# Kernel tuning notes

Measured on AMD Instinct MI355X. Metric: run time of the kernel, lower is better.

## Reference

```python
import jax, jax.numpy as jnp
import numpy as np

DIM = 384
B, H, W = 32, 32, 32


def setup_inputs() -> dict:
    key = jax.random.key(0)
    ks = jax.random.split(key, 10)
    s = 1.0 / np.sqrt(DIM)  # conv-like init scale
    return {
        "rgb_feat": jax.random.normal(ks[0], (B, DIM, H, W), dtype=jnp.float32),
        "ms_feat": jax.random.normal(ks[1], (B, DIM, H, W), dtype=jnp.float32),
        "Wq": jax.random.normal(ks[2], (DIM, DIM), dtype=jnp.float32) * s,
        "bq": jax.random.normal(ks[3], (DIM,), dtype=jnp.float32) * s,
        "Wk": jax.random.normal(ks[4], (DIM, DIM), dtype=jnp.float32) * s,
        "bk": jax.random.normal(ks[5], (DIM,), dtype=jnp.float32) * s,
        "Wv": jax.random.normal(ks[6], (DIM, DIM), dtype=jnp.float32) * s,
        "bv": jax.random.normal(ks[7], (DIM,), dtype=jnp.float32) * s,
        "Wf": jax.random.normal(ks[8], (DIM, DIM), dtype=jnp.float32) * s,
        "bf": jax.random.normal(ks[9], (DIM,), dtype=jnp.float32) * s,
    }


def _proj(x_bcn, Wdc, b_d):
    # 1x1 conv == channel-mixing linear: (b,c,n) -> (b,d,n)
    return jnp.einsum('dc,bcn->bdn', Wdc, x_bcn) + b_d[None, :, None]


def reference(rgb_feat, ms_feat, Wq, bq, Wk, bk, Wv, bv, Wf, bf):
    b, c, h, w = rgb_feat.shape
    n = h * w
    rgb = rgb_feat.reshape(b, c, n)
    ms = ms_feat.reshape(b, c, n)

    q = _proj(rgb, Wq, bq)   # (b, c, n)
    k = _proj(ms, Wk, bk)    # (b, c, n)
    v = _proj(ms, Wv, bv)    # (b, c, n)

    scale = 1.0 / jnp.sqrt(jnp.asarray(c, dtype=q.dtype))
    # scores: (b, n_q, n_k) == bmm(q^T, k) / sqrt(c)
    scores = jnp.einsum('bcn,bcm->bnm', q, k) * scale
    attn = jax.nn.softmax(scores, axis=-1)
    # out: (b, n, c) == bmm(attn, v^T); back to (b, c, n)
    out = jnp.einsum('bnm,bcm->bcn', attn, v)

    fused = _proj(out, Wf, bf)  # final 1x1 conv
    return fused.reshape(b, c, h, w)
```

## Files before the change

### kernel.cpp

```cpp
#include <hip/hip_runtime.h>

#define DIMC 384
#define NTOK 1024
#define BATCH 32
#define KT12 12

using short8 = __attribute__((ext_vector_type(8))) short;
using f32x4  = __attribute__((ext_vector_type(4))) float;
using uint4_ = __attribute__((ext_vector_type(4))) unsigned int;
typedef unsigned short u16;

#define MFMA16 __builtin_amdgcn_mfma_f32_16x16x32_bf16

#define GLD_LDS16(gp, lp)                                                     \
    __builtin_amdgcn_global_load_lds(                                         \
        (const __attribute__((address_space(1))) void*)(gp),                  \
        (__attribute__((address_space(3))) void*)(lp), 16, 0, 0)

__device__ __forceinline__ u16 f2bf(float f) {
    unsigned int u = __builtin_bit_cast(unsigned int, f);
    u += 0x7FFFu + ((u >> 16) & 1u);
    return (u16)(u >> 16);
}
__device__ __forceinline__ float bf2f(u16 h) {
    unsigned int u = ((unsigned int)h) << 16;
    return __builtin_bit_cast(float, u);
}


__global__ __launch_bounds__(256) void transpose_sw(
    const float* __restrict__ X0, u16* __restrict__ X0sw,
    const float* __restrict__ X1, u16* __restrict__ X1sw)
{
    __shared__ float tl[64 * 65];
    const int z = blockIdx.z;
    const float* X = (z < BATCH) ? X0 : X1;
    u16* Xsw = (z < BATCH) ? X0sw : X1sw;
    const int b = z & 31, n0 = blockIdx.x * 64, c0 = blockIdx.y * 64;
    const int t = threadIdx.x;

#pragma unroll
    for (int p = 0; p < 4; ++p) {
        int idx = p * 256 + t;
        int c = idx >> 4, n4 = (idx & 15) * 4;
        f32x4 v = *(const f32x4*)(X + ((size_t)b * DIMC + c0 + c) * NTOK + n0 + n4);
#pragma unroll
        for (int i = 0; i < 4; ++i) tl[c * 65 + n4 + i] = v[i];
    }
    __syncthreads();
    u16* dstb = Xsw + (size_t)b * NTOK * DIMC;
#pragma unroll
    for (int p = 0; p < 2; ++p) {
        int g = p * 256 + t;
        int n15 = g & 15, quad = (g >> 4) & 3, ktl = (g >> 6) & 1, rg = g >> 7;
        int c8 = ktl * 32 + quad * 8;
        int nl = rg * 16 + n15;
        uint4_ pk;
#pragma unroll
        for (int i = 0; i < 4; ++i) {
            u16 lo = f2bf(tl[(c8 + 2 * i) * 65 + nl]);
            u16 hi = f2bf(tl[(c8 + 2 * i + 1) * 65 + nl]);
            pk[i] = (unsigned)lo | ((unsigned)hi << 16);
        }
        size_t dst = (((size_t)(n0 >> 4) + rg) * KT12 + (c0 >> 5) + ktl) * 512 + (size_t)(g & 63) * 8;
        *(uint4_*)(dstb + dst) = pk;
    }
}

__global__ __launch_bounds__(256) void wcvt_sw(
    const float* __restrict__ w0, const float* __restrict__ w1,
    const float* __restrict__ w2, const float* __restrict__ w3,
    u16* __restrict__ dst, float s0)
{
    const float* srcs[4] = {w0, w1, w2, w3};
    const float* s = srcs[blockIdx.y];
    float scl = (blockIdx.y == 0) ? s0 : 1.0f;
    u16* d = dst + (size_t)blockIdx.y * DIMC * DIMC;
    int e0 = (blockIdx.x * 256 + threadIdx.x) * 8;
    int dd = e0 / DIMC, c8 = e0 % DIMC;
    f32x4 a = *(const f32x4*)(s + e0);
    f32x4 b2 = *(const f32x4*)(s + e0 + 4);
    uint4_ pk;
    pk[0] = (unsigned)f2bf(a[0] * scl) | ((unsigned)f2bf(a[1] * scl) << 16);
    pk[1] = (unsigned)f2bf(a[2] * scl) | ((unsigned)f2bf(a[3] * scl) << 16);
    pk[2] = (unsigned)f2bf(b2[0] * scl) | ((unsigned)f2bf(b2[1] * scl) << 16);
    pk[3] = (unsigned)f2bf(b2[2] * scl) | ((unsigned)f2bf(b2[3] * scl) << 16);
    size_t off = ((size_t)(dd >> 4) * KT12 + (c8 >> 5)) * 512 +
                 (size_t)((((c8 >> 3) & 3) * 16 + (dd & 15)) * 8);
    *(uint4_*)(d + off) = pk;
}

__global__ __launch_bounds__(256, 4) void proj3_g(
    const u16* __restrict__ rgb_sw, const u16* __restrict__ ms_sw,
    const u16* __restrict__ w_sw,
    u16* __restrict__ q_sw, u16* __restrict__ k_sw, u16* __restrict__ v_sw,
    const float* __restrict__ bq, const float* __restrict__ bk,
    const float* __restrict__ bv, float s0)
{
    __shared__ __align__(16) u16 smem[16384];

    const int bid = blockIdx.x;
    const int b = bid & 31;
    const int rr = bid >> 5;
    const int s = rr % 3, tile = rr / 3;
    const size_t TB = (size_t)NTOK * DIMC, WN = (size_t)DIMC * DIMC;
    const u16 *A, *B; u16* O; const float* bias;
    int ktd, bRow, r0, c0; float bsc = 1.f;
    if (s == 0) {
        A = rgb_sw + b * TB; B = w_sw; O = q_sw + b * TB; bias = bq;
        ktd = 12; bRow = 0; r0 = (tile & 7) * 128; c0 = (tile >> 3) * 128; bsc = s0;
    } else if (s == 1) {
        A = ms_sw + b * TB; B = w_sw + WN; O = k_sw + b * TB; bias = bk;
        ktd = 12; bRow = 0; r0 = (tile & 7) * 128; c0 = (tile >> 3) * 128;
    } else {
        A = w_sw + 2 * WN; B = ms_sw + b * TB; O = v_sw + b * TB; bias = bv;
        ktd = 32; bRow = 1; r0 = (tile % 3) * 128; c0 = (tile / 3) * 128;
    }

    const int t = threadIdx.x, w = t >> 6, lane = t & 63;
    const int l15 = lane & 15, quad = lane >> 4;
    const int wr = w >> 1, wc = w & 1;
    const int rt0 = r0 >> 4, ct0 = c0 >> 4;

    f32x4 acc[4][4];
#pragma unroll
    for (int ai = 0; ai < 4; ++ai)
#pragma unroll
        for (int bj = 0; bj < 4; ++bj) acc[ai][bj] = (f32x4){0.f, 0.f, 0.f, 0.f};

    {
        const u16* As = A + ((size_t)(rt0 + 2 * w) * KT12) * 512 + (size_t)lane * 8;
        GLD_LDS16(As, smem + (2 * w) * 512);
        GLD_LDS16(As + KT12 * 512, smem + (2 * w + 1) * 512);
        const u16* Bs = B + ((size_t)(ct0 + 2 * w) * KT12) * 512 + (size_t)lane * 8;
        GLD_LDS16(Bs, smem + 8192 + (2 * w) * 512);
        GLD_LDS16(Bs + KT12 * 512, smem + 8192 + (2 * w + 1) * 512);
    }
    __syncthreads();

    for (int kt = 0; kt < 12; ++kt) {
        const int cur = kt & 1;
        if (kt < 11) {
            u16* dA = smem + (cur ^ 1) * 4096;
            u16* dB = smem + 8192 + (cur ^ 1) * 4096;
            const u16* As = A + ((size_t)(rt0 + 2 * w) * KT12 + kt + 1) * 512 + (size_t)lane * 8;
            GLD_LDS16(As, dA + (2 * w) * 512);
            GLD_LDS16(As + KT12 * 512, dA + (2 * w + 1) * 512);
            const u16* Bs = B + ((size_t)(ct0 + 2 * w) * KT12 + kt + 1) * 512 + (size_t)lane * 8;
            GLD_LDS16(Bs, dB + (2 * w) * 512);
            GLD_LDS16(Bs + KT12 * 512, dB + (2 * w + 1) * 512);
        }
        const u16* sA = smem + cur * 4096 + (size_t)(wr * 4) * 512 + (size_t)lane * 8;
        const u16* sB = smem + 8192 + cur * 4096 + (size_t)(wc * 4) * 512 + (size_t)lane * 8;
        short8 aF[4], bF[4];
#pragma unroll
        for (int ai = 0; ai < 4; ++ai) aF[ai] = *(const short8*)(sA + ai * 512);
#pragma unroll
        for (int bj = 0; bj < 4; ++bj) bF[bj] = *(const short8*)(sB + bj * 512);
        __builtin_amdgcn_s_setprio(1);
#pragma unroll
        for (int ai = 0; ai < 4; ++ai)
#pragma unroll
            for (int bj = 0; bj < 4; ++bj)
                acc[ai][bj] = MFMA16(aF[ai], bF[bj], acc[ai][bj], 0, 0, 0);
        __builtin_amdgcn_s_setprio(0);
        __syncthreads();
    }
    u16* pw = smem + w * 1216;

    if (bRow) {
#pragma unroll
        for (int ai = 0; ai < 4; ++ai) {
            f32x4 bv4 = *(const f32x4*)(bias + r0 + wr * 64 + ai * 16 + quad * 4);
#pragma unroll
            for (int bj = 0; bj < 4; ++bj)
#pragma unroll
                for (int r = 0; r < 4; ++r) acc[ai][bj][r] += bv4[r];
        }
    } else {
#pragma unroll
        for (int bj = 0; bj < 4; ++bj) {
            float bc = bias[c0 + wc * 64 + bj * 16 + l15] * bsc;
#pragma unroll
            for (int ai = 0; ai < 4; ++ai)
#pragma unroll
                for (int r = 0; r < 4; ++r) acc[ai][bj][r] += bc;
        }
    }

#pragma unroll
    for (int ai = 0; ai < 4; ++ai) {
#pragma unroll
        for (int bj = 0; bj < 4; ++bj)
#pragma unroll
            for (int r = 0; r < 4; ++r)
                pw[(quad * 4 + r) * 76 + bj * 16 + l15] = f2bf(acc[ai][bj][r]);
        const int rt = rt0 + wr * 4 + ai;
        const int kb0 = (c0 + wc * 64) >> 5;
#pragma unroll
        for (int ktl = 0; ktl < 2; ++ktl) {
            uint4_ v = *(const uint4_*)(pw + l15 * 76 + ktl * 32 + quad * 8);
            *(uint4_*)(O + ((size_t)rt * ktd + kb0 + ktl) * 512 + (size_t)lane * 8) = v;
        }
    }
}

__global__ __launch_bounds__(256, 4) void projf_g(
    const u16* __restrict__ wf_sw, const u16* __restrict__ osw,
    const float* __restrict__ bfp, float* __restrict__ out)
{
    __shared__ __align__(16) u16 smem[16384];
    const int bid = blockIdx.x;
    const int b = bid & 31, tile = bid >> 5;
    const int r0 = (tile % 3) * 128, c0 = (tile / 3) * 128;
    const size_t TB = (size_t)NTOK * DIMC;

    const int t = threadIdx.x, w = t >> 6, lane = t & 63;
    const int l15 = lane & 15, quad = lane >> 4;
    const int wr = w >> 1, wc = w & 1;
    const int rt0 = r0 >> 4, ct0 = c0 >> 4;
    const u16* A = wf_sw;
    const u16* B = osw + (size_t)b * TB;

    f32x4 acc[4][4];
#pragma unroll
    for (int ai = 0; ai < 4; ++ai)
#pragma unroll
        for (int bj = 0; bj < 4; ++bj) acc[ai][bj] = (f32x4){0.f, 0.f, 0.f, 0.f};

    {
        const u16* As = A + ((size_t)(rt0 + 2 * w) * KT12) * 512 + (size_t)lane * 8;
        GLD_LDS16(As, smem + (2 * w) * 512);
        GLD_LDS16(As + KT12 * 512, smem + (2 * w + 1) * 512);
        const u16* Bs = B + ((size_t)(ct0 + 2 * w) * KT12) * 512 + (size_t)lane * 8;
        GLD_LDS16(Bs, smem + 8192 + (2 * w) * 512);
        GLD_LDS16(Bs + KT12 * 512, smem + 8192 + (2 * w + 1) * 512);
    }
    __syncthreads();

    for (int kt = 0; kt < 12; ++kt) {
        const int cur = kt & 1;
        if (kt < 11) {
            u16* dA = smem + (cur ^ 1) * 4096;
            u16* dB = smem + 8192 + (cur ^ 1) * 4096;
            const u16* As = A + ((size_t)(rt0 + 2 * w) * KT12 + kt + 1) * 512 + (size_t)lane * 8;
            GLD_LDS16(As, dA + (2 * w) * 512);
            GLD_LDS16(As + KT12 * 512, dA + (2 * w + 1) * 512);
            const u16* Bs = B + ((size_t)(ct0 + 2 * w) * KT12 + kt + 1) * 512 + (size_t)lane * 8;
            GLD_LDS16(Bs, dB + (2 * w) * 512);
            GLD_LDS16(Bs + KT12 * 512, dB + (2 * w + 1) * 512);
        }
        const u16* sA = smem + cur * 4096 + (size_t)(wr * 4) * 512 + (size_t)lane * 8;
        const u16* sB = smem + 8192 + cur * 4096 + (size_t)(wc * 4) * 512 + (size_t)lane * 8;
        short8 aF[4], bF[4];
#pragma unroll
        for (int ai = 0; ai < 4; ++ai) aF[ai] = *(const short8*)(sA + ai * 512);
#pragma unroll
        for (int bj = 0; bj < 4; ++bj) bF[bj] = *(const short8*)(sB + bj * 512);
        __builtin_amdgcn_s_setprio(1);
#pragma unroll
        for (int ai = 0; ai < 4; ++ai)
#pragma unroll
            for (int bj = 0; bj < 4; ++bj)
                acc[ai][bj] = MFMA16(aF[ai], bF[bj], acc[ai][bj], 0, 0, 0);
        __builtin_amdgcn_s_setprio(0);
        __syncthreads();
    }

    float* Ob = out + (size_t)b * DIMC * NTOK;
#pragma unroll
    for (int ai = 0; ai < 4; ++ai) {
        f32x4 bv4 = *(const f32x4*)(bfp + r0 + wr * 64 + ai * 16 + quad * 4);
#pragma unroll
        for (int bj = 0; bj < 4; ++bj) {
            const int col = c0 + wc * 64 + bj * 16 + l15;
#pragma unroll
            for (int r = 0; r < 4; ++r) {
                const int row = r0 + wr * 64 + ai * 16 + quad * 4 + r;
                Ob[(size_t)row * NTOK + col] = acc[ai][bj][r] + bv4[r];
            }
        }
    }
}

__global__ __launch_bounds__(512, 2) void attn_skew(
    const u16* __restrict__ qsw, const u16* __restrict__ ksw,
    const u16* __restrict__ vsw, u16* __restrict__ osw)
{
    __shared__ __align__(16) u16 smem[71168];

    const int bid = blockIdx.x;
    const int b = (bid & 7) * 4 + ((bid >> 3) & 3);
    const int qb = bid >> 5;
    const int t = threadIdx.x, w = t >> 6, lane = t & 63;
    const int l15 = lane & 15, quad = lane >> 4;
    const int rt = qb * 8 + w;

    const size_t TB = (size_t)NTOK * DIMC;
    const u16* kb = ksw + (size_t)b * TB;
    const u16* vb = vsw + (size_t)b * TB;
    u16* pw = smem + 61440 + w * 1216;

    short8 qf[12];
    const u16* qp = qsw + (size_t)b * TB + (size_t)rt * (KT12 * 512) + (size_t)lane * 8;
#pragma unroll
    for (int dk = 0; dk < 12; ++dk) qf[dk] = *(const short8*)(qp + dk * 512);

    f32x4 Oa[24];
#pragma unroll
    for (int i = 0; i < 24; ++i) Oa[i] = (f32x4){0.f, 0.f, 0.f, 0.f};
    float m_run[4], l_run[4];
#pragma unroll
    for (int r = 0; r < 4; ++r) { m_run[r] = -1e30f; l_run[r] = 0.f; }

    const int i0 = w * 3;

#pragma unroll
    for (int j = 0; j < 3; ++j) {
        int idx = i0 + j;
        GLD_LDS16(kb + (size_t)idx * 512 + lane * 8, smem + idx * 512);
        GLD_LDS16(kb + (size_t)(24 + idx) * 512 + lane * 8, smem + 12288 + idx * 512);
        GLD_LDS16(vb + (size_t)(idx * 32) * 512 + lane * 8, smem + 36864 + idx * 512);
    }
    __syncthreads();

    f32x4 s0[2], s1[2];
    {
        s0[0] = (f32x4){0.f, 0.f, 0.f, 0.f};
        s0[1] = (f32x4){0.f, 0.f, 0.f, 0.f};
        const u16* kfb = smem + (size_t)lane * 8;
        __builtin_amdgcn_s_setprio(1);
#pragma unroll
        for (int dk = 0; dk < 12; ++dk) {
            short8 k0 = *(const short8*)(kfb + dk * 512);
            short8 k1 = *(const short8*)(kfb + (12 + dk) * 512);
            s0[0] = MFMA16(qf[dk], k0, s0[0], 0, 0, 0);
            s0[1] = MFMA16(qf[dk], k1, s0[1], 0, 0, 0);
        }
        __builtin_amdgcn_s_setprio(0);
    }

    auto body = [&](int mt, f32x4 (&SC)[2], f32x4 (&SP)[2], int qkb, int dmb) {
        if (mt < 30) {
            u16* kd = smem + dmb * 12288;
            const u16* ks = kb + (size_t)(24 * (mt + 2)) * 512 + (size_t)lane * 8;
#pragma unroll
            for (int j = 0; j < 3; ++j) {
                int idx = i0 + j;
                GLD_LDS16(ks + (size_t)idx * 512, kd + idx * 512);
            }
        }
        if (mt < 31) {
            u16* vd = smem + 36864 + ((mt + 1) & 1) * 12288;
            const u16* vs = vb + (size_t)(mt + 1) * 512 + (size_t)lane * 8;
#pragma unroll
            for (int j = 0; j < 3; ++j) {
                int idx = i0 + j;
                GLD_LDS16(vs + (size_t)(idx * 32) * 512, vd + idx * 512);
            }
            SP[0] = (f32x4){0.f, 0.f, 0.f, 0.f};
            SP[1] = (f32x4){0.f, 0.f, 0.f, 0.f};
            const u16* kfb = smem + qkb * 12288 + (size_t)lane * 8;
            __builtin_amdgcn_s_setprio(1);
#pragma unroll
            for (int dk = 0; dk < 12; ++dk) {
                short8 k0 = *(const short8*)(kfb + dk * 512);
                short8 k1 = *(const short8*)(kfb + (12 + dk) * 512);
                SP[0] = MFMA16(qf[dk], k0, SP[0], 0, 0, 0);
                SP[1] = MFMA16(qf[dk], k1, SP[1], 0, 0, 0);
            }
            __builtin_amdgcn_s_setprio(0);
        }

        float mx4[4];
#pragma unroll
        for (int r = 0; r < 4; ++r) {
            float mx = fmaxf(SC[0][r], SC[1][r]);
            mx = fmaxf(mx, __shfl_xor(mx, 1));
            mx = fmaxf(mx, __shfl_xor(mx, 2));
            mx = fmaxf(mx, __shfl_xor(mx, 4));
            mx = fmaxf(mx, __shfl_xor(mx, 8));
            mx4[r] = mx;
        }
        int grow = (mx4[0] > m_run[0] + 8.f) | (mx4[1] > m_run[1] + 8.f) |
                   (mx4[2] > m_run[2] + 8.f) | (mx4[3] > m_run[3] + 8.f);
        if (__any(grow)) {
            float alpha[4];
#pragma unroll
            for (int r = 0; r < 4; ++r) {
                float mn = fmaxf(m_run[r], mx4[r]);
                alpha[r] = exp2f(m_run[r] - mn);
                m_run[r] = mn;
                l_run[r] *= alpha[r];
            }
#pragma unroll
            for (int ci = 0; ci < 24; ++ci)
#pragma unroll
                for (int r = 0; r < 4; ++r) Oa[ci][r] *= alpha[r];
        }
#pragma unroll
        for (int r = 0; r < 4; ++r) {
            float ls = 0.f;
#pragma unroll
            for (int mc = 0; mc < 2; ++mc) {
                float p = exp2f(SC[mc][r] - m_run[r]);
                u16 pb = f2bf(p);
                pw[(quad * 4 + r) * 76 + mc * 16 + l15] = pb;
                ls += bf2f(pb);
            }
            ls += __shfl_xor(ls, 1);
            ls += __shfl_xor(ls, 2);
            ls += __shfl_xor(ls, 4);
            ls += __shfl_xor(ls, 8);
            l_run[r] += ls;
        }

        short8 pa = *(const short8*)(pw + l15 * 76 + quad * 8);
        const u16* vfb = smem + 36864 + (mt & 1) * 12288 + (size_t)lane * 8;
        __builtin_amdgcn_s_setprio(1);
#pragma unroll
        for (int ci = 0; ci < 24; ++ci) {
            short8 vf = *(const short8*)(vfb + ci * 512);
            Oa[ci] = MFMA16(pa, vf, Oa[ci], 0, 0, 0);
        }
        __builtin_amdgcn_s_setprio(0);

        __syncthreads();
    };

    int b0 = 0, b1 = 1, b2 = 2;
    for (int tp = 0; tp < 16; ++tp) {
        const int mt = 2 * tp;
        body(mt, s0, s1, b1, b2);
        body(mt + 1, s1, s0, b2, b0);
        int tmp = b0; b0 = b2; b2 = b1; b1 = tmp;
    }

    float rl[4];
#pragma unroll
    for (int r = 0; r < 4; ++r) rl[r] = 1.f / l_run[r];
    u16* od = osw + (size_t)b * TB;
#pragma unroll
    for (int ch = 0; ch < 6; ++ch) {
#pragma unroll
        for (int cc = 0; cc < 4; ++cc)
#pragma unroll
            for (int r = 0; r < 4; ++r)
                pw[(quad * 4 + r) * 76 + cc * 16 + l15] = f2bf(Oa[ch * 4 + cc][r] * rl[r]);
#pragma unroll
        for (int ktl = 0; ktl < 2; ++ktl) {
            uint4_ vv = *(const uint4_*)(pw + l15 * 76 + ktl * 32 + quad * 8);
            size_t dst = ((size_t)rt * KT12 + ch * 2 + ktl) * 512 + (size_t)lane * 8;
            *(uint4_*)(od + dst) = vv;
        }
    }
}

extern "C" void kernel_launch(void* const* d_in, const int* in_sizes, int n_in,
                              void* d_out, int out_size, void* d_ws, size_t ws_size,
                              hipStream_t stream) {
    const float* rgb = (const float*)d_in[0];
    const float* ms  = (const float*)d_in[1];
    const float* Wq  = (const float*)d_in[2];
    const float* bq  = (const float*)d_in[3];
    const float* Wk  = (const float*)d_in[4];
    const float* bk  = (const float*)d_in[5];
    const float* Wv  = (const float*)d_in[6];
    const float* bv  = (const float*)d_in[7];
    const float* Wf  = (const float*)d_in[8];
    const float* bf_ = (const float*)d_in[9];
    float* outp = (float*)d_out;

    const float SC2 = 0.05103103630798288f * 1.4426950408889634f;

    const size_t TN = (size_t)BATCH * NTOK * DIMC;
    const size_t WN = (size_t)DIMC * DIMC;
    u16* rgb_sw = (u16*)d_ws;
    u16* ms_sw  = rgb_sw + TN;
    u16* q_sw   = ms_sw + TN;
    u16* k_sw   = q_sw + TN;
    u16* v_sw   = k_sw + TN;
    u16* o_sw   = v_sw + TN;
    u16* w_sw   = o_sw + TN;

    wcvt_sw<<<dim3(72, 4), 256, 0, stream>>>(Wq, Wk, Wv, Wf, w_sw, SC2);
    transpose_sw<<<dim3(16, 6, 2 * BATCH), 256, 0, stream>>>(rgb, rgb_sw, ms, ms_sw);

    proj3_g<<<dim3(2304), 256, 0, stream>>>(
        rgb_sw, ms_sw, w_sw, q_sw, k_sw, v_sw, bq, bk, bv, SC2);

    attn_skew<<<dim3(256), 512, 0, stream>>>(q_sw, k_sw, v_sw, o_sw);

    projf_g<<<dim3(768), 256, 0, stream>>>(w_sw + 3 * WN, o_sw, bf_, outp);
}
```

Before: 329.8 us.

## Replace skewed QK/PV attention pipeline with single-stage loop using partial vmcnt waits

```diff
diff --git a/kernel.cpp b/kernel.cpp
--- a/kernel.cpp
+++ b/kernel.cpp
@@ -283,7 +283,7 @@
     }
 }
 
-__global__ __launch_bounds__(512, 2) void attn_skew(
+__global__ __launch_bounds__(512, 2) void attn_t4(
     const u16* __restrict__ qsw, const u16* __restrict__ ksw,
     const u16* __restrict__ vsw, u16* __restrict__ osw)
 {
@@ -318,64 +318,68 @@
 #pragma unroll
     for (int j = 0; j < 3; ++j) {
         int idx = i0 + j;
+        GLD_LDS16(vb + (size_t)(idx * 32) * 512 + lane * 8, smem + 36864 + idx * 512);
+    }
+#pragma unroll
+    for (int j = 0; j < 3; ++j) {
+        int idx = i0 + j;
         GLD_LDS16(kb + (size_t)idx * 512 + lane * 8, smem + idx * 512);
+    }
+#pragma unroll
+    for (int j = 0; j < 3; ++j) {
+        int idx = i0 + j;
         GLD_LDS16(kb + (size_t)(24 + idx) * 512 + lane * 8, smem + 12288 + idx * 512);
-        GLD_LDS16(vb + (size_t)(idx * 32) * 512 + lane * 8, smem + 36864 + idx * 512);
-    }
-    __syncthreads();
-
-    f32x4 s0[2], s1[2];
-    {
-        s0[0] = (f32x4){0.f, 0.f, 0.f, 0.f};
-        s0[1] = (f32x4){0.f, 0.f, 0.f, 0.f};
-        const u16* kfb = smem + (size_t)lane * 8;
+    }
+
+    for (int mt = 0; mt < 32; ++mt) {
+        if (mt < 31) {
+            asm volatile("s_waitcnt vmcnt(3)" ::: "memory");
+        } else {
+            asm volatile("s_waitcnt vmcnt(0)" ::: "memory");
+        }
+        __builtin_amdgcn_s_barrier();
+        __builtin_amdgcn_sched_barrier(0);
+
+        if (mt < 31) {
+            u16* vnxt = smem + 36864 + ((mt + 1) & 1) * 12288;
+            const u16* vs = vb + (size_t)(mt + 1) * 512 + (size_t)lane * 8;
+#pragma unroll
+            for (int j = 0; j < 3; ++j) {
+                int idx = i0 + j;
+                GLD_LDS16(vs + (size_t)(idx * 32) * 512, vnxt + idx * 512);
+            }
+        }
+        if (mt < 30) {
+            u16* knxt = smem + ((mt + 2) % 3) * 12288;
+            const u16* ks = kb + (size_t)(24 * (mt + 2)) * 512 + (size_t)lane * 8;
+#pragma unroll
+            for (int j = 0; j < 3; ++j) {
+                int idx = i0 + j;
+                GLD_LDS16(ks + (size_t)idx * 512, knxt + idx * 512);
+            }
+        }
+
+        const u16* kcur = smem + (mt % 3) * 12288;
+        const u16* vcur = smem + 36864 + (mt & 1) * 12288;
+
+        f32x4 s[2];
+        s[0] = (f32x4){0.f, 0.f, 0.f, 0.f};
+        s[1] = (f32x4){0.f, 0.f, 0.f, 0.f};
+        const u16* kfb = kcur + (size_t)lane * 8;
         __builtin_amdgcn_s_setprio(1);
 #pragma unroll
         for (int dk = 0; dk < 12; ++dk) {
             short8 k0 = *(const short8*)(kfb + dk * 512);
             short8 k1 = *(const short8*)(kfb + (12 + dk) * 512);
-            s0[0] = MFMA16(qf[dk], k0, s0[0], 0, 0, 0);
-            s0[1] = MFMA16(qf[dk], k1, s0[1], 0, 0, 0);
+            s[0] = MFMA16(qf[dk], k0, s[0], 0, 0, 0);
+            s[1] = MFMA16(qf[dk], k1, s[1], 0, 0, 0);
         }
         __builtin_amdgcn_s_setprio(0);
-    }
-
-    auto body = [&](int mt, f32x4 (&SC)[2], f32x4 (&SP)[2], int qkb, int dmb) {
-        if (mt < 30) {
-            u16* kd = smem + dmb * 12288;
-            const u16* ks = kb + (size_t)(24 * (mt + 2)) * 512 + (size_t)lane * 8;
-#pragma unroll
-            for (int j = 0; j < 3; ++j) {
-                int idx = i0 + j;
-                GLD_LDS16(ks + (size_t)idx * 512, kd + idx * 512);
-            }
-        }
-        if (mt < 31) {
-            u16* vd = smem + 36864 + ((mt + 1) & 1) * 12288;
-            const u16* vs = vb + (size_t)(mt + 1) * 512 + (size_t)lane * 8;
-#pragma unroll
-            for (int j = 0; j < 3; ++j) {
-                int idx = i0 + j;
-                GLD_LDS16(vs + (size_t)(idx * 32) * 512, vd + idx * 512);
-            }
-            SP[0] = (f32x4){0.f, 0.f, 0.f, 0.f};
-            SP[1] = (f32x4){0.f, 0.f, 0.f, 0.f};
-            const u16* kfb = smem + qkb * 12288 + (size_t)lane * 8;
-            __builtin_amdgcn_s_setprio(1);
-#pragma unroll
-            for (int dk = 0; dk < 12; ++dk) {
-                short8 k0 = *(const short8*)(kfb + dk * 512);
-                short8 k1 = *(const short8*)(kfb + (12 + dk) * 512);
-                SP[0] = MFMA16(qf[dk], k0, SP[0], 0, 0, 0);
-                SP[1] = MFMA16(qf[dk], k1, SP[1], 0, 0, 0);
-            }
-            __builtin_amdgcn_s_setprio(0);
-        }
 
         float mx4[4];
 #pragma unroll
         for (int r = 0; r < 4; ++r) {
-            float mx = fmaxf(SC[0][r], SC[1][r]);
+            float mx = fmaxf(s[0][r], s[1][r]);
             mx = fmaxf(mx, __shfl_xor(mx, 1));
             mx = fmaxf(mx, __shfl_xor(mx, 2));
             mx = fmaxf(mx, __shfl_xor(mx, 4));
@@ -403,7 +407,7 @@
             float ls = 0.f;
 #pragma unroll
             for (int mc = 0; mc < 2; ++mc) {
-                float p = exp2f(SC[mc][r] - m_run[r]);
+                float p = exp2f(s[mc][r] - m_run[r]);
                 u16 pb = f2bf(p);
                 pw[(quad * 4 + r) * 76 + mc * 16 + l15] = pb;
                 ls += bf2f(pb);
@@ -416,7 +420,7 @@
         }
 
         short8 pa = *(const short8*)(pw + l15 * 76 + quad * 8);
-        const u16* vfb = smem + 36864 + (mt & 1) * 12288 + (size_t)lane * 8;
+        const u16* vfb = vcur + (size_t)lane * 8;
         __builtin_amdgcn_s_setprio(1);
 #pragma unroll
         for (int ci = 0; ci < 24; ++ci) {
@@ -424,16 +428,6 @@
             Oa[ci] = MFMA16(pa, vf, Oa[ci], 0, 0, 0);
         }
         __builtin_amdgcn_s_setprio(0);
-
-        __syncthreads();
-    };
-
-    int b0 = 0, b1 = 1, b2 = 2;
-    for (int tp = 0; tp < 16; ++tp) {
-        const int mt = 2 * tp;
-        body(mt, s0, s1, b1, b2);
-        body(mt + 1, s1, s0, b2, b0);
-        int tmp = b0; b0 = b2; b2 = b1; b1 = tmp;
     }
 
     float rl[4];
@@ -489,7 +483,7 @@
     proj3_g<<<dim3(2304), 256, 0, stream>>>(
         rgb_sw, ms_sw, w_sw, q_sw, k_sw, v_sw, bq, bk, bv, SC2);
 
-    attn_skew<<<dim3(256), 512, 0, stream>>>(q_sw, k_sw, v_sw, o_sw);
+    attn_t4<<<dim3(256), 512, 0, stream>>>(q_sw, k_sw, v_sw, o_sw);
 
     projf_g<<<dim3(768), 256, 0, stream>>>(w_sw + 3 * WN, o_sw, bf_, outp);
 }
```

Result: slower. 341.8 us (+3.6%).
